# Optimization experiments

Measured on AMD Instinct MI355X. Metric: run time of the kernel, lower is better.

The kernel has to match this reference:

```python
import jax, jax.numpy as jnp
import numpy as np

B, T, E, U, V = 64, 100, 512, 512, 32000


def gru_layer(xs_tm, Wg, bg, Wc, bc):
    """TF GRUCell math. xs_tm: [T, B, D]. Returns (ys [T,B,U], h_final [B,U])."""
    u_dim = Wc.shape[1]
    h0 = jnp.zeros((xs_tm.shape[1], u_dim), xs_tm.dtype)

    def step(h, x):
        ru = jax.nn.sigmoid(jnp.concatenate([x, h], -1) @ Wg + bg)
        r, u = jnp.split(ru, 2, axis=-1)
        c = jnp.tanh(jnp.concatenate([x, r * h], -1) @ Wc + bc)
        h_new = u * h + (1.0 - u) * c
        return h_new, h_new

    h_final, ys = jax.lax.scan(step, h0, xs_tm)
    return ys, h_final


def setup_inputs() -> dict:
    key = jax.random.key(0)
    ks = jax.random.split(key, 16)

    def w(k, shape):
        fan_in = shape[0]
        return jax.random.normal(k, shape, jnp.float32) * (1.0 / np.sqrt(fan_in))

    inp = {
        "x": jax.random.randint(ks[0], (B, T), 0, V, jnp.int32),
        "embedding": jax.random.normal(ks[1], (V, E), jnp.float32) * 0.02,
        # bi-directional layer, input dim E
        "Wg_fw": w(ks[2], (E + U, 2 * U)), "bg_fw": jnp.ones((2 * U,), jnp.float32),
        "Wc_fw": w(ks[3], (E + U, U)),     "bc_fw": jnp.zeros((U,), jnp.float32),
        "Wg_bw": w(ks[4], (E + U, 2 * U)), "bg_bw": jnp.ones((2 * U,), jnp.float32),
        "Wc_bw": w(ks[5], (E + U, U)),     "bc_bw": jnp.zeros((U,), jnp.float32),
        # uni layer 1, input dim 2U (concat fw/bw)
        "Wg_u1": w(ks[6], (2 * U + U, 2 * U)), "bg_u1": jnp.ones((2 * U,), jnp.float32),
        "Wc_u1": w(ks[7], (2 * U + U, U)),     "bc_u1": jnp.zeros((U,), jnp.float32),
        # uni layer 2, input dim U
        "Wg_u2": w(ks[8], (U + U, 2 * U)), "bg_u2": jnp.ones((2 * U,), jnp.float32),
        "Wc_u2": w(ks[9], (U + U, U)),     "bc_u2": jnp.zeros((U,), jnp.float32),
    }
    return inp


def reference(x, embedding, Wg_fw, bg_fw, Wc_fw, bc_fw, Wg_bw, bg_bw, Wc_bw, bc_bw,
              Wg_u1, bg_u1, Wc_u1, bc_u1, Wg_u2, bg_u2, Wc_u2, bc_u2):
    emb = embedding[x]                      # [B, T, E] embedding lookup
    xs = jnp.swapaxes(emb, 0, 1)            # [T, B, E] time-major for scan
    # bidirectional GRU layer
    yf, _ = gru_layer(xs, Wg_fw, bg_fw, Wc_fw, bc_fw)
    yb, _ = gru_layer(xs[::-1], Wg_bw, bg_bw, Wc_bw, bc_bw)
    a = jnp.concatenate([yf, yb[::-1]], -1)  # [T, B, 2U]
    # 2-layer unidirectional GRU stack (MultiRNNCell)
    a, s1 = gru_layer(a, Wg_u1, bg_u1, Wc_u1, bc_u1)
    a, s2 = gru_layer(a, Wg_u2, bg_u2, Wc_u2, bc_u2)
    output = jnp.swapaxes(a, 0, 1)          # [B, T, U]
    state = jnp.stack([s1, s2])             # [2, B, U] per-layer final states
    return output, state
```

## Files before the change

### kernel.cpp

```cpp
#include <hip/hip_runtime.h>
#include <hip/hip_bf16.h>


#define TT 100

using f32x4 = __attribute__((ext_vector_type(4))) float;
using s16x8 = __attribute__((ext_vector_type(8))) short;
using u32x4 = __attribute__((ext_vector_type(4))) unsigned;

__device__ __forceinline__ unsigned short f2bfu(float x) {
  __hip_bfloat16 b = __float2bfloat16(x);
  unsigned short u;
  __builtin_memcpy(&u, &b, sizeof(u));
  return u;
}
__device__ __forceinline__ float bfu2f(unsigned short u) {
  __hip_bfloat16 b;
  __builtin_memcpy(&b, &u, sizeof(b));
  return __bfloat162float(b);
}
__device__ __forceinline__ float sigm(float x) {
  x = fminf(fmaxf(x, -30.f), 30.f);
  return 1.f / (1.f + __expf(-x));
}
__device__ __forceinline__ float tanh_fast(float x) {
  x = fminf(fmaxf(x, -15.f), 15.f);
  float e = __expf(-2.f * x);
  return (1.f - e) / (1.f + e);
}
__device__ __forceinline__ void vm_drain() {
  asm volatile("s_waitcnt vmcnt(0)" ::: "memory");
}
__device__ __forceinline__ void sc1_store_b16(void* p, unsigned v) {
  asm volatile("global_store_short %0, %1, off sc0 sc1" :: "v"(p), "v"(v) : "memory");
}

__global__ __launch_bounds__(256) void pack_w_kernel(const float* __restrict__ Wg,
                                                     const float* __restrict__ Wc,
                                                     int ldg, int ldc, int ktTot,
                                                     unsigned short* __restrict__ hi,
                                                     unsigned short* __restrict__ lo) {
  const int gg = blockIdx.x * 256 + threadIdx.x;
  if (gg >= 96 * ktTot * 64) return;
  const int lane = gg & 63;
  const int pair = gg >> 6;
  const int kt = pair % ktTot;
  const int nt = pair / ktTot;
  const int kg = lane >> 4;
  const int nl = lane & 15;
  const size_t off = (size_t)gg * 8;
  for (int i = 0; i < 8; ++i) {
    const int k = kt * 32 + kg * 8 + i;
    float v = (nt < 64) ? Wg[(size_t)k * ldg + nt * 16 + nl]
                        : Wc[(size_t)k * ldc + (nt - 64) * 16 + nl];
    unsigned short h = f2bfu(v);
    hi[off + i] = h;
    lo[off + i] = f2bfu(v - bfu2f(h));
  }
}

template <int ASRC>
__global__ __launch_bounds__(256) void gemm_mfma(
    const int* __restrict__ xtok, const float* __restrict__ emb,
    const unsigned short* __restrict__ aHi, const unsigned short* __restrict__ aLo, int lda,
    const unsigned short* __restrict__ bHi, const unsigned short* __restrict__ bLo,
    int ktTot, int ktX,
    const float* __restrict__ bg, const float* __restrict__ bc,
    float* __restrict__ C) {
  __shared__ unsigned short Ah[128 * 40];
  __shared__ unsigned short Al[128 * 40];

  const int tid = threadIdx.x;
  const int lane = tid & 63;
  const int w = tid >> 6;
  const int bm = blockIdx.x, bn = blockIdx.y;
  const int fm = lane & 15, fkg = lane >> 4;

  const int arow = tid >> 1;
  const int koff = (tid & 1) * 16;
  const int rowg = bm * 128 + arow;
  int embIdx = 0;
  if (ASRC == 0) {
    const int t_ = rowg >> 6, b_ = rowg & 63;
    embIdx = xtok[b_ * TT + t_];
  }

  f32x4 acc[2][8];
#pragma unroll
  for (int rt = 0; rt < 2; ++rt)
#pragma unroll
    for (int ni = 0; ni < 8; ++ni) acc[rt][ni] = (f32x4){0.f, 0.f, 0.f, 0.f};

  for (int kt = 0; kt < ktX; ++kt) {
    __syncthreads();
    if (ASRC == 0) {
      const float* src = emb + (size_t)embIdx * 512 + kt * 32 + koff;
      s16x8 h0, h1, l0, l1;
#pragma unroll
      for (int c = 0; c < 2; ++c) {
        f32x4 va = *(const f32x4*)(src + c * 8);
        f32x4 vb = *(const f32x4*)(src + c * 8 + 4);
        s16x8 hh, ll;
#pragma unroll
        for (int j = 0; j < 4; ++j) {
          unsigned short h = f2bfu(va[j]);
          hh[j] = (short)h; ll[j] = (short)f2bfu(va[j] - bfu2f(h));
          unsigned short h2 = f2bfu(vb[j]);
          hh[j + 4] = (short)h2; ll[j + 4] = (short)f2bfu(vb[j] - bfu2f(h2));
        }
        if (c == 0) { h0 = hh; l0 = ll; } else { h1 = hh; l1 = ll; }
      }
      *(s16x8*)(Ah + arow * 40 + koff) = h0;
      *(s16x8*)(Ah + arow * 40 + koff + 8) = h1;
      *(s16x8*)(Al + arow * 40 + koff) = l0;
      *(s16x8*)(Al + arow * 40 + koff + 8) = l1;
    } else {
      const size_t so = (size_t)rowg * lda + kt * 32 + koff;
      s16x8 h0 = *(const s16x8*)(aHi + so);
      s16x8 h1 = *(const s16x8*)(aHi + so + 8);
      s16x8 l0 = *(const s16x8*)(aLo + so);
      s16x8 l1 = *(const s16x8*)(aLo + so + 8);
      *(s16x8*)(Ah + arow * 40 + koff) = h0;
      *(s16x8*)(Ah + arow * 40 + koff + 8) = h1;
      *(s16x8*)(Al + arow * 40 + koff) = l0;
      *(s16x8*)(Al + arow * 40 + koff + 8) = l1;
    }
    __syncthreads();

    s16x8 ah[2], al[2];
#pragma unroll
    for (int rt = 0; rt < 2; ++rt) {
      const int m = w * 32 + rt * 16 + fm;
      ah[rt] = *(const s16x8*)(Ah + m * 40 + fkg * 8);
      al[rt] = *(const s16x8*)(Al + m * 40 + fkg * 8);
    }
#pragma unroll
    for (int ni = 0; ni < 8; ++ni) {
      const int nt = bn * 8 + ni;
      const size_t bo = ((size_t)nt * ktTot + kt) * 512 + lane * 8;
      s16x8 bh = *(const s16x8*)(bHi + bo);
      s16x8 bl = *(const s16x8*)(bLo + bo);
#pragma unroll
      for (int rt = 0; rt < 2; ++rt) {
        acc[rt][ni] = __builtin_amdgcn_mfma_f32_16x16x32_bf16(ah[rt], bh, acc[rt][ni], 0, 0, 0);
        acc[rt][ni] = __builtin_amdgcn_mfma_f32_16x16x32_bf16(ah[rt], bl, acc[rt][ni], 0, 0, 0);
        acc[rt][ni] = __builtin_amdgcn_mfma_f32_16x16x32_bf16(al[rt], bh, acc[rt][ni], 0, 0, 0);
      }
    }
  }

#pragma unroll
  for (int ni = 0; ni < 8; ++ni) {
    const int nt = bn * 8 + ni;
    int dcol; float bias;
    if (nt < 64) { dcol = nt * 16 + fm; bias = bg[dcol]; }
    else { dcol = 1024 + (nt - 64) * 16 + fm; bias = bc[(nt - 64) * 16 + fm]; }
#pragma unroll
    for (int rt = 0; rt < 2; ++rt)
#pragma unroll
      for (int j = 0; j < 4; ++j) {
        const int row = bm * 128 + w * 32 + rt * 16 + fkg * 4 + j;
        C[(size_t)row * 1536 + dcol] = acc[rt][ni][j] + bias;
      }
  }
}

template <int NB>
__global__ __launch_bounds__(256, 1) void gru_scan_kernel(
    const float* __restrict__ gxF, const float* __restrict__ gxB,
    const unsigned short* __restrict__ wHiF, const unsigned short* __restrict__ wLoF,
    const unsigned short* __restrict__ wHiB, const unsigned short* __restrict__ wLoB,
    int ktTot, int ktH0,
    unsigned* __restrict__ hPkG, unsigned* __restrict__ rPkG,
    unsigned* __restrict__ slots,
    unsigned short* __restrict__ yHi, unsigned short* __restrict__ yLo, int yld,
    float* __restrict__ outb,
    float* __restrict__ stout) {
  __shared__ unsigned short wHi_s[3 * 8192];
  __shared__ unsigned short wLo_s[3 * 8192];
  __shared__ float scr[4][16][17];
  __shared__ float scr2[4][16][17];

  const int tid = threadIdx.x;
  const int lane = tid & 63;
  const int wv = tid >> 6;
  const int bid = blockIdx.x;
  const int g = bid & 7;
  const int wg = bid >> 3;
  const int hs = wg << 4;

  int dir = 0, b0;
  const float* gx;
  const unsigned short *wph, *wpl;
  if (NB == 16) {
    dir = g & 1;
    b0 = (g >> 1) << 4;
    gx = dir ? gxB : gxF;
    wph = dir ? wHiB : wHiF;
    wpl = dir ? wLoB : wLoF;
  } else {
    b0 = g * NB;
    gx = gxF;
    wph = wHiF;
    wpl = wLoF;
  }

  {
    const int nt0[3] = {wg, 32 + wg, 64 + wg};
    for (int c = 0; c < 3; ++c) {
      const unsigned short* sH = wph + ((size_t)nt0[c] * ktTot + ktH0) * 512;
      const unsigned short* sL = wpl + ((size_t)nt0[c] * ktTot + ktH0) * 512;
      unsigned short* dH = wHi_s + c * 8192;
      unsigned short* dL = wLo_s + c * 8192;
#pragma unroll
      for (int it = 0; it < 4; ++it) {
        const int o = (it * 256 + tid) * 8;
        *(s16x8*)(dH + o) = *(const s16x8*)(sH + o);
        *(s16x8*)(dL + o) = *(const s16x8*)(sL + o);
      }
    }
  }
  __syncthreads();

  unsigned* gslots = slots + g * 32;

  const int fm = lane & 15;
  const int fkg = lane >> 4;
  const int afe = fm * 512;
  const int asw = (fm & 7) << 3;

  const int ob = tid >> 4, oj = tid & 15;
  const bool own = (ob < NB);
  const int ui = ob * 512 + ((hs + oj) ^ ((ob & 7) << 3));

  const size_t tileo = (size_t)g * 8192;

  auto mfma_regs = [&](int cidx, const s16x8* ah, const s16x8* al,
                       float (*dst)[16][17]) {
    f32x4 acc0 = {0.f, 0.f, 0.f, 0.f}, acc1 = {0.f, 0.f, 0.f, 0.f};
#pragma unroll
    for (int q = 0; q < 4; ++q) {
      const int kt = wv * 4 + q;
      const int wo = ((cidx * 16 + kt) * 64 + lane) * 8;
      s16x8 bh = *(const s16x8*)(wHi_s + wo);
      s16x8 bl = *(const s16x8*)(wLo_s + wo);
      if (q & 1) {
        acc1 = __builtin_amdgcn_mfma_f32_16x16x32_bf16(ah[q], bh, acc1, 0, 0, 0);
        acc1 = __builtin_amdgcn_mfma_f32_16x16x32_bf16(ah[q], bl, acc1, 0, 0, 0);
        acc1 = __builtin_amdgcn_mfma_f32_16x16x32_bf16(al[q], bh, acc1, 0, 0, 0);
      } else {
        acc0 = __builtin_amdgcn_mfma_f32_16x16x32_bf16(ah[q], bh, acc0, 0, 0, 0);
        acc0 = __builtin_amdgcn_mfma_f32_16x16x32_bf16(ah[q], bl, acc0, 0, 0, 0);
        acc0 = __builtin_amdgcn_mfma_f32_16x16x32_bf16(al[q], bh, acc0, 0, 0, 0);
      }
    }
#pragma unroll
    for (int j = 0; j < 4; ++j) dst[wv][fkg * 4 + j][fm] = acc0[j] + acc1[j];
  };

  auto load_frags = [&](const unsigned* pk, s16x8* ah, s16x8* al,
                        bool withHv, unsigned* hvOut) {
    u32x4 d[4][2];
#pragma unroll
    for (int q = 0; q < 4; ++q) {
      const int kt = wv * 4 + q;
      const unsigned* p = pk + tileo + afe + ((kt * 32 + fkg * 8) ^ asw);
      asm volatile("global_load_dwordx4 %0, %1, off sc0 sc1"
                   : "=v"(d[q][0]) : "v"(p) : "memory");
      asm volatile("global_load_dwordx4 %0, %1, off sc0 sc1"
                   : "=v"(d[q][1]) : "v"(p + 4) : "memory");
    }
    if (withHv && own)
      asm volatile("global_load_dword %0, %1, off sc0 sc1"
                   : "=v"(*hvOut) : "v"(pk + tileo + ui) : "memory");
    vm_drain();
    __builtin_amdgcn_sched_barrier(0);
#pragma unroll
    for (int q = 0; q < 4; ++q) {
      u32x4 hh, ll;
#pragma unroll
      for (int i = 0; i < 2; ++i) {
        const u32x4 dd = d[q][i];
        hh[2 * i] = (dd[0] & 0xffffu) | (dd[1] << 16);
        hh[2 * i + 1] = (dd[2] & 0xffffu) | (dd[3] << 16);
        ll[2 * i] = (dd[0] >> 16) | (dd[1] & 0xffff0000u);
        ll[2 * i + 1] = (dd[2] >> 16) | (dd[3] & 0xffff0000u);
      }
      __builtin_memcpy(&ah[q], &hh, 16);
      __builtin_memcpy(&al[q], &ll, 16);
    }
  };

  auto poll = [&](unsigned target) {
    if (tid < 32) {
      const unsigned* p = gslots + tid;
      unsigned v;
      do {
        asm volatile("global_load_dword %0, %1, off sc0 sc1\n\ts_waitcnt vmcnt(0)"
                     : "=v"(v) : "v"(p) : "memory");
      } while (!__all(v >= target));
    }
    __syncthreads();
  };

  float gxr = 0.f, gxu = 0.f, gxc = 0.f;
  if (own) {
    const float* row = gx + ((size_t)(dir ? TT - 1 : 0) * 64 + b0 + ob) * 1536 + hs + oj;
    gxr = row[0]; gxu = row[512]; gxc = row[1024];
  }

  for (int t = 0; t < TT; ++t) {
    const int tg = dir ? (TT - 1 - t) : t;

    s16x8 ah[4], al[4];
    unsigned hvu = 0;
    load_frags(hPkG, ah, al, true, &hvu);
    mfma_regs(0, ah, al, scr);
    __syncthreads();

    float hv = 0.f;
    if (own) {
      float rpre = scr[0][ob][oj] + scr[1][ob][oj] + scr[2][ob][oj] + scr[3][ob][oj] + gxr;
      float sg = sigm(rpre);
      hv = bfu2f((unsigned short)(hvu & 0xffffu)) + bfu2f((unsigned short)(hvu >> 16));
      float rh = sg * hv;
      unsigned short hh_ = f2bfu(rh);
      unsigned short ll_ = f2bfu(rh - bfu2f(hh_));
      unsigned e = (unsigned)hh_ | ((unsigned)ll_ << 16);
      asm volatile("global_store_dword %0, %1, off sc0 sc1"
                   :: "v"(rPkG + tileo + ui), "v"(e) : "memory");
    }
    vm_drain();
    __syncthreads();
    if (tid == 0) {
      unsigned tv = 2 * t + 1;
      asm volatile("global_store_dword %0, %1, off sc0 sc1"
                   :: "v"(gslots + wg), "v"(tv) : "memory");
    }

    mfma_regs(1, ah, al, scr2);

    float ngxr = 0.f, ngxu = 0.f, ngxc = 0.f;
    if (own && t + 1 < TT) {
      const int tgn = dir ? (TT - 2 - t) : (t + 1);
      const float* row = gx + ((size_t)tgn * 64 + b0 + ob) * 1536 + hs + oj;
      ngxr = row[0]; ngxu = row[512]; ngxc = row[1024];
    }

    poll(2 * t + 1);

    load_frags(rPkG, ah, al, false, nullptr);
    mfma_regs(2, ah, al, scr);
    __syncthreads();

    float hn = 0.f;
    unsigned short hh_ = 0, ll_ = 0;
    if (own) {
      float upre = scr2[0][ob][oj] + scr2[1][ob][oj] + scr2[2][ob][oj] + scr2[3][ob][oj] + gxu;
      float uv = sigm(upre);
      float cpre = scr[0][ob][oj] + scr[1][ob][oj] + scr[2][ob][oj] + scr[3][ob][oj] + gxc;
      float cv = tanh_fast(cpre);
      hn = uv * hv + (1.f - uv) * cv;
      hh_ = f2bfu(hn);
      ll_ = f2bfu(hn - bfu2f(hh_));
    }

    if (t == TT - 1) {
      if (own) {
        if (yHi) {
          const int ycol = (NB == 16) ? (dir * 512 + hs + oj) : (hs + oj);
          const size_t yi = ((size_t)tg * 64 + (b0 + ob)) * yld + ycol;
          yHi[yi] = hh_; yLo[yi] = ll_;
        }
        if (outb) outb[((size_t)(b0 + ob) * TT + t) * 512 + hs + oj] = hn;
        if (stout) stout[(size_t)(b0 + ob) * 512 + hs + oj] = hn;
      }
      break;
    }

    if (own) {
      unsigned e = (unsigned)hh_ | ((unsigned)ll_ << 16);
      asm volatile("global_store_dword %0, %1, off sc0 sc1"
                   :: "v"(hPkG + tileo + ui), "v"(e) : "memory");
    }
    vm_drain();
    __syncthreads();
    if (tid == 0) {
      unsigned tv = 2 * t + 2;
      asm volatile("global_store_dword %0, %1, off sc0 sc1"
                   :: "v"(gslots + wg), "v"(tv) : "memory");
    }

    if (own) {
      if (yHi) {
        const int ycol = (NB == 16) ? (dir * 512 + hs + oj) : (hs + oj);
        const size_t yi = ((size_t)tg * 64 + (b0 + ob)) * yld + ycol;
        yHi[yi] = hh_; yLo[yi] = ll_;
      }
      if (outb) outb[((size_t)(b0 + ob) * TT + t) * 512 + hs + oj] = hn;
    }
    gxr = ngxr; gxu = ngxu; gxc = ngxc;

    poll(2 * t + 2);
  }
}

__global__ __launch_bounds__(256, 1) void uni_fused_kernel(
    const float* __restrict__ gx1,
    const unsigned short* __restrict__ w1Hi, const unsigned short* __restrict__ w1Lo,
    const unsigned short* __restrict__ w2Hi, const unsigned short* __restrict__ w2Lo,
    const float* __restrict__ bg2, const float* __restrict__ bc2,
    unsigned* __restrict__ hPk1, unsigned* __restrict__ rPk1,
    unsigned* __restrict__ hPk2, unsigned* __restrict__ rPk2,
    unsigned* __restrict__ slots1, unsigned* __restrict__ slots2,
    unsigned short* __restrict__ y1Hi, unsigned short* __restrict__ y1Lo,
    float* __restrict__ out, float* __restrict__ st1, float* __restrict__ st2) {
  __shared__ unsigned short wHi_s[3 * 8192];
  __shared__ unsigned short wLo_s[3 * 8192];
  __shared__ float scr[4][16][17];
  __shared__ float scr2[4][16][17];
  __shared__ float scr3[4][16][17];

  const int tid = threadIdx.x;
  const int lane = tid & 63;
  const int wv = tid >> 6;
  const int bid = blockIdx.x;
  const int role = (bid >= 128);
  const int g = (bid & 127) >> 5;
  const int wg = bid & 31;
  const int hs = wg << 4;
  const int b0 = g * 16;

  const unsigned short* wph = role ? w2Hi : w1Hi;
  const unsigned short* wpl = role ? w2Lo : w1Lo;
  const int ktTot = role ? 32 : 48;
  const int ktH0 = role ? 16 : 32;
  unsigned* hPk = role ? hPk2 : hPk1;
  unsigned* rPk = role ? rPk2 : rPk1;
  unsigned* myslots = (role ? slots2 : slots1) + g * 32;
  unsigned* u1gs = slots1 + g * 32;

  {
    const int nt0[3] = {wg, 32 + wg, 64 + wg};
    for (int c = 0; c < 3; ++c) {
      const unsigned short* sH = wph + ((size_t)nt0[c] * ktTot + ktH0) * 512;
      const unsigned short* sL = wpl + ((size_t)nt0[c] * ktTot + ktH0) * 512;
      unsigned short* dH = wHi_s + c * 8192;
      unsigned short* dL = wLo_s + c * 8192;
#pragma unroll
      for (int it = 0; it < 4; ++it) {
        const int o = (it * 256 + tid) * 8;
        *(s16x8*)(dH + o) = *(const s16x8*)(sH + o);
        *(s16x8*)(dL + o) = *(const s16x8*)(sL + o);
      }
    }
  }
  __syncthreads();

  const int fm = lane & 15;
  const int fkg = lane >> 4;
  const int afe = fm * 512;
  const int asw = (fm & 7) << 3;
  const int ob = tid >> 4, oj = tid & 15;
  const int ui = ob * 512 + ((hs + oj) ^ ((ob & 7) << 3));
  const size_t tileo = (size_t)g * 8192;

  auto mfma_regs = [&](int cidx, const s16x8* ah, const s16x8* al,
                       float (*dst)[16][17]) {
    f32x4 acc0 = {0.f, 0.f, 0.f, 0.f}, acc1 = {0.f, 0.f, 0.f, 0.f};
#pragma unroll
    for (int q = 0; q < 4; ++q) {
      const int kt = wv * 4 + q;
      const int wo = ((cidx * 16 + kt) * 64 + lane) * 8;
      s16x8 bh = *(const s16x8*)(wHi_s + wo);
      s16x8 bl = *(const s16x8*)(wLo_s + wo);
      if (q & 1) {
        acc1 = __builtin_amdgcn_mfma_f32_16x16x32_bf16(ah[q], bh, acc1, 0, 0, 0);
        acc1 = __builtin_amdgcn_mfma_f32_16x16x32_bf16(ah[q], bl, acc1, 0, 0, 0);
        acc1 = __builtin_amdgcn_mfma_f32_16x16x32_bf16(al[q], bh, acc1, 0, 0, 0);
      } else {
        acc0 = __builtin_amdgcn_mfma_f32_16x16x32_bf16(ah[q], bh, acc0, 0, 0, 0);
        acc0 = __builtin_amdgcn_mfma_f32_16x16x32_bf16(ah[q], bl, acc0, 0, 0, 0);
        acc0 = __builtin_amdgcn_mfma_f32_16x16x32_bf16(al[q], bh, acc0, 0, 0, 0);
      }
    }
#pragma unroll
    for (int j = 0; j < 4; ++j) dst[wv][fkg * 4 + j][fm] = acc0[j] + acc1[j];
  };

  auto mfma_xp = [&](int cidx, const s16x8* ah, const s16x8* al,
                     float (*dst)[16][17]) {
    const int nt0[3] = {wg, 32 + wg, 64 + wg};
    f32x4 acc0 = {0.f, 0.f, 0.f, 0.f}, acc1 = {0.f, 0.f, 0.f, 0.f};
#pragma unroll
    for (int q = 0; q < 4; ++q) {
      const int kt = wv * 4 + q;
      const size_t bo = ((size_t)nt0[cidx] * 32 + kt) * 512 + lane * 8;
      s16x8 bh = *(const s16x8*)(w2Hi + bo);
      s16x8 bl = *(const s16x8*)(w2Lo + bo);
      if (q & 1) {
        acc1 = __builtin_amdgcn_mfma_f32_16x16x32_bf16(ah[q], bh, acc1, 0, 0, 0);
        acc1 = __builtin_amdgcn_mfma_f32_16x16x32_bf16(ah[q], bl, acc1, 0, 0, 0);
        acc1 = __builtin_amdgcn_mfma_f32_16x16x32_bf16(al[q], bh, acc1, 0, 0, 0);
      } else {
        acc0 = __builtin_amdgcn_mfma_f32_16x16x32_bf16(ah[q], bh, acc0, 0, 0, 0);
        acc0 = __builtin_amdgcn_mfma_f32_16x16x32_bf16(ah[q], bl, acc0, 0, 0, 0);
        acc0 = __builtin_amdgcn_mfma_f32_16x16x32_bf16(al[q], bh, acc0, 0, 0, 0);
      }
    }
#pragma unroll
    for (int j = 0; j < 4; ++j) dst[wv][fkg * 4 + j][fm] = acc0[j] + acc1[j];
  };

  auto load_frags = [&](const unsigned* pk, s16x8* ah, s16x8* al,
                        bool withHv, unsigned* hvOut) {
    u32x4 d[4][2];
#pragma unroll
    for (int q = 0; q < 4; ++q) {
      const int kt = wv * 4 + q;
      const unsigned* p = pk + tileo + afe + ((kt * 32 + fkg * 8) ^ asw);
      asm volatile("global_load_dwordx4 %0, %1, off sc0 sc1"
                   : "=v"(d[q][0]) : "v"(p) : "memory");
      asm volatile("global_load_dwordx4 %0, %1, off sc0 sc1"
                   : "=v"(d[q][1]) : "v"(p + 4) : "memory");
    }
    if (withHv)
      asm volatile("global_load_dword %0, %1, off sc0 sc1"
                   : "=v"(*hvOut) : "v"(pk + tileo + ui) : "memory");
    vm_drain();
    __builtin_amdgcn_sched_barrier(0);
#pragma unroll
    for (int q = 0; q < 4; ++q) {
      u32x4 hh, ll;
#pragma unroll
      for (int i = 0; i < 2; ++i) {
        const u32x4 dd = d[q][i];
        hh[2 * i] = (dd[0] & 0xffffu) | (dd[1] << 16);
        hh[2 * i + 1] = (dd[2] & 0xffffu) | (dd[3] << 16);
        ll[2 * i] = (dd[0] >> 16) | (dd[1] & 0xffff0000u);
        ll[2 * i + 1] = (dd[2] >> 16) | (dd[3] & 0xffff0000u);
      }
      __builtin_memcpy(&ah[q], &hh, 16);
      __builtin_memcpy(&al[q], &ll, 16);
    }
  };

  auto poll_arr = [&](const unsigned* arr, unsigned target) {
    if (tid < 32) {
      const unsigned* p = arr + tid;
      unsigned v;
      do {
        asm volatile("global_load_dword %0, %1, off sc0 sc1\n\ts_waitcnt vmcnt(0)"
                     : "=v"(v) : "v"(p) : "memory");
      } while (!__all(v >= target));
    }
    __syncthreads();
  };

  if (role == 0) {
    float gxr, gxu, gxc;
    {
      const float* row = gx1 + ((size_t)0 * 64 + b0 + ob) * 1536 + hs + oj;
      gxr = row[0]; gxu = row[512]; gxc = row[1024];
    }
    for (int t = 0; t < TT; ++t) {
      s16x8 ah[4], al[4];
      unsigned hvu = 0;
      load_frags(hPk, ah, al, true, &hvu);
      mfma_regs(0, ah, al, scr);
      __syncthreads();

      float rpre = scr[0][ob][oj] + scr[1][ob][oj] + scr[2][ob][oj] + scr[3][ob][oj] + gxr;
      float sg = sigm(rpre);
      float hv = bfu2f((unsigned short)(hvu & 0xffffu)) + bfu2f((unsigned short)(hvu >> 16));
      float rh = sg * hv;
      {
        unsigned short hh_ = f2bfu(rh);
        unsigned short ll_ = f2bfu(rh - bfu2f(hh_));
        unsigned e = (unsigned)hh_ | ((unsigned)ll_ << 16);
        asm volatile("global_store_dword %0, %1, off sc0 sc1"
                     :: "v"(rPk + tileo + ui), "v"(e) : "memory");
      }
      vm_drain();
      __syncthreads();
      if (tid == 0) {
        unsigned tv = 2 * t + 1;
        asm volatile("global_store_dword %0, %1, off sc0 sc1"
                     :: "v"(myslots + wg), "v"(tv) : "memory");
      }

      mfma_regs(1, ah, al, scr2);

      float ngxr = 0.f, ngxu = 0.f, ngxc = 0.f;
      if (t + 1 < TT) {
        const float* row = gx1 + ((size_t)(t + 1) * 64 + b0 + ob) * 1536 + hs + oj;
        ngxr = row[0]; ngxu = row[512]; ngxc = row[1024];
      }

      poll_arr(myslots, 2 * t + 1);

      load_frags(rPk, ah, al, false, nullptr);
      mfma_regs(2, ah, al, scr);
      __syncthreads();

      float upre = scr2[0][ob][oj] + scr2[1][ob][oj] + scr2[2][ob][oj] + scr2[3][ob][oj] + gxu;
      float uv = sigm(upre);
      float cpre = scr[0][ob][oj] + scr[1][ob][oj] + scr[2][ob][oj] + scr[3][ob][oj] + gxc;
      float hn = uv * hv + (1.f - uv) * tanh_fast(cpre);
      unsigned short hh_ = f2bfu(hn);
      unsigned short ll_ = f2bfu(hn - bfu2f(hh_));

      {
        const size_t yi = ((size_t)t * 64 + (b0 + ob)) * 512 + hs + oj;
        sc1_store_b16(y1Hi + yi, hh_);
        sc1_store_b16(y1Lo + yi, ll_);
      }
      if (t < TT - 1) {
        unsigned e = (unsigned)hh_ | ((unsigned)ll_ << 16);
        asm volatile("global_store_dword %0, %1, off sc0 sc1"
                     :: "v"(hPk + tileo + ui), "v"(e) : "memory");
      } else {
        st1[(size_t)(b0 + ob) * 512 + hs + oj] = hn;
      }
      vm_drain();
      __syncthreads();
      if (tid == 0) {
        unsigned tv = 2 * t + 2;
        asm volatile("global_store_dword %0, %1, off sc0 sc1"
                     :: "v"(myslots + wg), "v"(tv) : "memory");
      }
      if (t == TT - 1) break;
      gxr = ngxr; gxu = ngxu; gxc = ngxc;
      poll_arr(myslots, 2 * t + 2);
    }
  } else {
    const float br = bg2[hs + oj], bu = bg2[512 + hs + oj], bc_ = bc2[hs + oj];
    for (int t = 0; t < TT; ++t) {
      poll_arr(u1gs, 2 * t + 2);

      s16x8 xh[4], xl[4];
      {
#pragma unroll
        for (int q = 0; q < 4; ++q) {
          const int kt = wv * 4 + q;
          const size_t yo = ((size_t)t * 64 + b0 + fm) * 512 + kt * 32 + fkg * 8;
          asm volatile("global_load_dwordx4 %0, %1, off sc0 sc1"
                       : "=v"(xh[q]) : "v"(y1Hi + yo) : "memory");
          asm volatile("global_load_dwordx4 %0, %1, off sc0 sc1"
                       : "=v"(xl[q]) : "v"(y1Lo + yo) : "memory");
        }
        vm_drain();
        __builtin_amdgcn_sched_barrier(0);
      }
      mfma_xp(0, xh, xl, scr);
      mfma_xp(1, xh, xl, scr2);
      mfma_xp(2, xh, xl, scr3);
      __syncthreads();
      float gxr = scr[0][ob][oj] + scr[1][ob][oj] + scr[2][ob][oj] + scr[3][ob][oj] + br;
      float gxu = scr2[0][ob][oj] + scr2[1][ob][oj] + scr2[2][ob][oj] + scr2[3][ob][oj] + bu;
      float gxc = scr3[0][ob][oj] + scr3[1][ob][oj] + scr3[2][ob][oj] + scr3[3][ob][oj] + bc_;
      __syncthreads();

      s16x8 ah[4], al[4];
      unsigned hvu = 0;
      load_frags(hPk, ah, al, true, &hvu);
      mfma_regs(0, ah, al, scr);
      __syncthreads();

      float rpre = scr[0][ob][oj] + scr[1][ob][oj] + scr[2][ob][oj] + scr[3][ob][oj] + gxr;
      float sg = sigm(rpre);
      float hv = bfu2f((unsigned short)(hvu & 0xffffu)) + bfu2f((unsigned short)(hvu >> 16));
      float rh = sg * hv;
      {
        unsigned short hh_ = f2bfu(rh);
        unsigned short ll_ = f2bfu(rh - bfu2f(hh_));
        unsigned e = (unsigned)hh_ | ((unsigned)ll_ << 16);
        asm volatile("global_store_dword %0, %1, off sc0 sc1"
                     :: "v"(rPk + tileo + ui), "v"(e) : "memory");
      }
      vm_drain();
      __syncthreads();
      if (tid == 0) {
        unsigned tv = 2 * t + 1;
        asm volatile("global_store_dword %0, %1, off sc0 sc1"
                     :: "v"(myslots + wg), "v"(tv) : "memory");
      }

      mfma_regs(1, ah, al, scr2);
      poll_arr(myslots, 2 * t + 1);

      load_frags(rPk, ah, al, false, nullptr);
      mfma_regs(2, ah, al, scr);
      __syncthreads();

      float upre = scr2[0][ob][oj] + scr2[1][ob][oj] + scr2[2][ob][oj] + scr2[3][ob][oj] + gxu;
      float uv = sigm(upre);
      float cpre = scr[0][ob][oj] + scr[1][ob][oj] + scr[2][ob][oj] + scr[3][ob][oj] + gxc;
      float hn = uv * hv + (1.f - uv) * tanh_fast(cpre);

      if (t == TT - 1) {
        out[((size_t)(b0 + ob) * TT + t) * 512 + hs + oj] = hn;
        st2[(size_t)(b0 + ob) * 512 + hs + oj] = hn;
        break;
      }
      {
        unsigned short hh_ = f2bfu(hn);
        unsigned short ll_ = f2bfu(hn - bfu2f(hh_));
        unsigned e = (unsigned)hh_ | ((unsigned)ll_ << 16);
        asm volatile("global_store_dword %0, %1, off sc0 sc1"
                     :: "v"(hPk + tileo + ui), "v"(e) : "memory");
      }
      vm_drain();
      __syncthreads();
      if (tid == 0) {
        unsigned tv = 2 * t + 2;
        asm volatile("global_store_dword %0, %1, off sc0 sc1"
                     :: "v"(myslots + wg), "v"(tv) : "memory");
      }
      out[((size_t)(b0 + ob) * TT + t) * 512 + hs + oj] = hn;
      poll_arr(myslots, 2 * t + 2);
    }
  }
}

extern "C" void kernel_launch(void* const* d_in, const int* in_sizes, int n_in,
                              void* d_out, int out_size, void* d_ws, size_t ws_size,
                              hipStream_t stream) {
  (void)in_sizes; (void)n_in; (void)out_size; (void)ws_size;
  const int* x = (const int*)d_in[0];
  const float* emb = (const float*)d_in[1];
  const float* WgFw = (const float*)d_in[2];
  const float* bgFw = (const float*)d_in[3];
  const float* WcFw = (const float*)d_in[4];
  const float* bcFw = (const float*)d_in[5];
  const float* WgBw = (const float*)d_in[6];
  const float* bgBw = (const float*)d_in[7];
  const float* WcBw = (const float*)d_in[8];
  const float* bcBw = (const float*)d_in[9];
  const float* WgU1 = (const float*)d_in[10];
  const float* bgU1 = (const float*)d_in[11];
  const float* WcU1 = (const float*)d_in[12];
  const float* bcU1 = (const float*)d_in[13];
  const float* WgU2 = (const float*)d_in[14];
  const float* bgU2 = (const float*)d_in[15];
  const float* WcU2 = (const float*)d_in[16];
  const float* bcU2 = (const float*)d_in[17];

  char* ws = (char*)d_ws;
  float* bufA = (float*)(ws + 0);
  float* bufB = (float*)(ws + 39321600);
  unsigned short* ycatHi = (unsigned short*)(ws + 78643200);
  unsigned short* ycatLo = (unsigned short*)(ws + 91750400);
  unsigned short* y1Hi = (unsigned short*)(ws + 78643200);
  unsigned short* y1Lo = (unsigned short*)(ws + 85196800);
  unsigned short* wpFwHi = (unsigned short*)(ws + 104857600);
  unsigned short* wpFwLo = (unsigned short*)(ws + 108003328);
  unsigned short* wpBwHi = (unsigned short*)(ws + 111149056);
  unsigned short* wpBwLo = (unsigned short*)(ws + 114294784);
  unsigned short* wpU1Hi = (unsigned short*)(ws + 117440512);
  unsigned short* wpU1Lo = (unsigned short*)(ws + 122159104);
  unsigned short* wpU2Hi = (unsigned short*)(ws + 104857600);
  unsigned short* wpU2Lo = (unsigned short*)(ws + 108003328);
  unsigned* tiles = (unsigned*)(ws + 126877696);
  unsigned* bars = (unsigned*)(ws + 127401984);

  unsigned* hPkB = tiles;
  unsigned* rPkB = tiles + 65536;
  unsigned* hPk1 = tiles;
  unsigned* rPk1 = tiles + 32768;
  unsigned* hPk2 = tiles + 65536;
  unsigned* rPk2 = tiles + 98304;

  float* out = (float*)d_out;
  float* st1 = out + (size_t)64 * TT * 512;
  float* st2 = st1 + 64 * 512;

  hipMemsetAsync(bars, 0, 4096, stream);

  pack_w_kernel<<<768, 256, 0, stream>>>(WgFw, WcFw, 1024, 512, 32, wpFwHi, wpFwLo);
  pack_w_kernel<<<768, 256, 0, stream>>>(WgBw, WcBw, 1024, 512, 32, wpBwHi, wpBwLo);
  pack_w_kernel<<<1152, 256, 0, stream>>>(WgU1, WcU1, 1024, 512, 48, wpU1Hi, wpU1Lo);

  gemm_mfma<0><<<dim3(50, 12), 256, 0, stream>>>(
      x, emb, nullptr, nullptr, 0, wpFwHi, wpFwLo, 32, 16, bgFw, bcFw, bufA);
  gemm_mfma<0><<<dim3(50, 12), 256, 0, stream>>>(
      x, emb, nullptr, nullptr, 0, wpBwHi, wpBwLo, 32, 16, bgBw, bcBw, bufB);

  hipMemsetAsync(tiles, 0, 524288, stream);
  {
    const float *a0 = bufA, *a1 = bufB;
    const unsigned short *w0 = wpFwHi, *w1 = wpFwLo, *w2 = wpBwHi, *w3 = wpBwLo;
    int ktT = 32, ktH = 16;
    unsigned *h0 = hPkB, *r0 = rPkB;
    unsigned* bp = bars;
    unsigned short *yh = ycatHi, *yl = ycatLo; int yld = 1024;
    float *on = nullptr, *sn = nullptr;
    void* args[] = {&a0, &a1, &w0, &w1, &w2, &w3, &ktT, &ktH, &h0, &r0,
                    &bp, &yh, &yl, &yld, &on, &sn};
    hipLaunchCooperativeKernel((const void*)gru_scan_kernel<16>, dim3(256), dim3(256),
                               args, 0, stream);
  }

  pack_w_kernel<<<768, 256, 0, stream>>>(WgU2, WcU2, 1024, 512, 32, wpU2Hi, wpU2Lo);

  gemm_mfma<1><<<dim3(50, 12), 256, 0, stream>>>(
      nullptr, nullptr, ycatHi, ycatLo, 1024, wpU1Hi, wpU1Lo, 48, 32, bgU1, bcU1, bufA);

  hipMemsetAsync(tiles, 0, 524288, stream);
  {
    const float* a0 = bufA;
    const unsigned short *w0 = wpU1Hi, *w1 = wpU1Lo, *w2 = wpU2Hi, *w3 = wpU2Lo;
    const float *b2 = bgU2, *c2 = bcU2;
    unsigned *h1 = hPk1, *r1 = rPk1, *h2 = hPk2, *r2 = rPk2;
    unsigned *s1p = bars + 256, *s2p = bars + 384;
    unsigned short *yh = y1Hi, *yl = y1Lo;
    float *op = out, *t1 = st1, *t2 = st2;
    void* args[] = {&a0, &w0, &w1, &w2, &w3, &b2, &c2,
                    &h1, &r1, &h2, &r2, &s1p, &s2p, &yh, &yl, &op, &t1, &t2};
    hipLaunchCooperativeKernel((const void*)uni_fused_kernel, dim3(256), dim3(256),
                               args, 0, stream);
  }
}
```

Measured before the change: 1.591 ms.

## Fuse embedding input projections into bidirectional scan and pipeline layer-2 projections

Drops the two standalone input-projection GEMMs for the bidirectional layer. The scan kernel now gathers embedding rows, splits them to hi/lo bf16 and computes the x·W gate projections per timestep with MFMA, overlapping them with waits on the recurrent barrier. The layer-2 scan also moves its next-step input projection into the current step's barrier wait slots. This removes the large gx buffer traffic and two kernel launches, but adds MFMA work and global weight reads to the latency-critical serial loop, plus extra block syncs.

```diff
diff --git a/kernel.cpp b/kernel.cpp
--- a/kernel.cpp
+++ b/kernel.cpp
@@ -79,11 +79,6 @@
   const int arow = tid >> 1;
   const int koff = (tid & 1) * 16;
   const int rowg = bm * 128 + arow;
-  int embIdx = 0;
-  if (ASRC == 0) {
-    const int t_ = rowg >> 6, b_ = rowg & 63;
-    embIdx = xtok[b_ * TT + t_];
-  }
 
   f32x4 acc[2][8];
 #pragma unroll
@@ -93,28 +88,7 @@
 
   for (int kt = 0; kt < ktX; ++kt) {
     __syncthreads();
-    if (ASRC == 0) {
-      const float* src = emb + (size_t)embIdx * 512 + kt * 32 + koff;
-      s16x8 h0, h1, l0, l1;
-#pragma unroll
-      for (int c = 0; c < 2; ++c) {
-        f32x4 va = *(const f32x4*)(src + c * 8);
-        f32x4 vb = *(const f32x4*)(src + c * 8 + 4);
-        s16x8 hh, ll;
-#pragma unroll
-        for (int j = 0; j < 4; ++j) {
-          unsigned short h = f2bfu(va[j]);
-          hh[j] = (short)h; ll[j] = (short)f2bfu(va[j] - bfu2f(h));
-          unsigned short h2 = f2bfu(vb[j]);
-          hh[j + 4] = (short)h2; ll[j + 4] = (short)f2bfu(vb[j] - bfu2f(h2));
-        }
-        if (c == 0) { h0 = hh; l0 = ll; } else { h1 = hh; l1 = ll; }
-      }
-      *(s16x8*)(Ah + arow * 40 + koff) = h0;
-      *(s16x8*)(Ah + arow * 40 + koff + 8) = h1;
-      *(s16x8*)(Al + arow * 40 + koff) = l0;
-      *(s16x8*)(Al + arow * 40 + koff + 8) = l1;
-    } else {
+    {
       const size_t so = (size_t)rowg * lda + kt * 32 + koff;
       s16x8 h0 = *(const s16x8*)(aHi + so);
       s16x8 h1 = *(const s16x8*)(aHi + so + 8);
@@ -165,21 +139,20 @@
   }
 }
 
-template <int NB>
-__global__ __launch_bounds__(256, 1) void gru_scan_kernel(
-    const float* __restrict__ gxF, const float* __restrict__ gxB,
+__global__ __launch_bounds__(256, 1) void bidir_scan_kernel(
+    const int* __restrict__ xtok, const float* __restrict__ emb,
     const unsigned short* __restrict__ wHiF, const unsigned short* __restrict__ wLoF,
     const unsigned short* __restrict__ wHiB, const unsigned short* __restrict__ wLoB,
-    int ktTot, int ktH0,
+    const float* __restrict__ bgF, const float* __restrict__ bcF,
+    const float* __restrict__ bgB, const float* __restrict__ bcB,
     unsigned* __restrict__ hPkG, unsigned* __restrict__ rPkG,
     unsigned* __restrict__ slots,
-    unsigned short* __restrict__ yHi, unsigned short* __restrict__ yLo, int yld,
-    float* __restrict__ outb,
-    float* __restrict__ stout) {
+    unsigned short* __restrict__ yHi, unsigned short* __restrict__ yLo) {
   __shared__ unsigned short wHi_s[3 * 8192];
   __shared__ unsigned short wLo_s[3 * 8192];
   __shared__ float scr[4][16][17];
   __shared__ float scr2[4][16][17];
+  __shared__ float scr3[4][16][17];
 
   const int tid = threadIdx.x;
   const int lane = tid & 63;
@@ -188,28 +161,19 @@
   const int g = bid & 7;
   const int wg = bid >> 3;
   const int hs = wg << 4;
-
-  int dir = 0, b0;
-  const float* gx;
-  const unsigned short *wph, *wpl;
-  if (NB == 16) {
-    dir = g & 1;
-    b0 = (g >> 1) << 4;
-    gx = dir ? gxB : gxF;
-    wph = dir ? wHiB : wHiF;
-    wpl = dir ? wLoB : wLoF;
-  } else {
-    b0 = g * NB;
-    gx = gxF;
-    wph = wHiF;
-    wpl = wLoF;
-  }
+  const int dir = g & 1;
+  const int b0 = (g >> 1) << 4;
+
+  const unsigned short* wph = dir ? wHiB : wHiF;
+  const unsigned short* wpl = dir ? wLoB : wLoF;
+  const float* bgD = dir ? bgB : bgF;
+  const float* bcD = dir ? bcB : bcF;
 
   {
     const int nt0[3] = {wg, 32 + wg, 64 + wg};
     for (int c = 0; c < 3; ++c) {
-      const unsigned short* sH = wph + ((size_t)nt0[c] * ktTot + ktH0) * 512;
-      const unsigned short* sL = wpl + ((size_t)nt0[c] * ktTot + ktH0) * 512;
+      const unsigned short* sH = wph + ((size_t)nt0[c] * 32 + 16) * 512;
+      const unsigned short* sL = wpl + ((size_t)nt0[c] * 32 + 16) * 512;
       unsigned short* dH = wHi_s + c * 8192;
       unsigned short* dL = wLo_s + c * 8192;
 #pragma unroll
@@ -223,17 +187,14 @@
   __syncthreads();
 
   unsigned* gslots = slots + g * 32;
-
   const int fm = lane & 15;
   const int fkg = lane >> 4;
   const int afe = fm * 512;
   const int asw = (fm & 7) << 3;
-
   const int ob = tid >> 4, oj = tid & 15;
-  const bool own = (ob < NB);
   const int ui = ob * 512 + ((hs + oj) ^ ((ob & 7) << 3));
-
   const size_t tileo = (size_t)g * 8192;
+  const float br = bgD[hs + oj], bu = bgD[512 + hs + oj], bcv = bcD[hs + oj];
 
   auto mfma_regs = [&](int cidx, const s16x8* ah, const s16x8* al,
                        float (*dst)[16][17]) {
@@ -258,6 +219,50 @@
     for (int j = 0; j < 4; ++j) dst[wv][fkg * 4 + j][fm] = acc0[j] + acc1[j];
   };
 
+  auto mfma_xpg = [&](int nt, const s16x8* xh, const s16x8* xl,
+                      float (*dst)[16][17]) {
+    f32x4 acc0 = {0.f, 0.f, 0.f, 0.f}, acc1 = {0.f, 0.f, 0.f, 0.f};
+#pragma unroll
+    for (int q = 0; q < 4; ++q) {
+      const int kt = wv * 4 + q;
+      const size_t bo = ((size_t)nt * 32 + kt) * 512 + lane * 8;
+      s16x8 bh = *(const s16x8*)(wph + bo);
+      s16x8 bl = *(const s16x8*)(wpl + bo);
+      if (q & 1) {
+        acc1 = __builtin_amdgcn_mfma_f32_16x16x32_bf16(xh[q], bh, acc1, 0, 0, 0);
+        acc1 = __builtin_amdgcn_mfma_f32_16x16x32_bf16(xh[q], bl, acc1, 0, 0, 0);
+        acc1 = __builtin_amdgcn_mfma_f32_16x16x32_bf16(xl[q], bh, acc1, 0, 0, 0);
+      } else {
+        acc0 = __builtin_amdgcn_mfma_f32_16x16x32_bf16(xh[q], bh, acc0, 0, 0, 0);
+        acc0 = __builtin_amdgcn_mfma_f32_16x16x32_bf16(xh[q], bl, acc0, 0, 0, 0);
+        acc0 = __builtin_amdgcn_mfma_f32_16x16x32_bf16(xl[q], bh, acc0, 0, 0, 0);
+      }
+    }
+#pragma unroll
+    for (int j = 0; j < 4; ++j) dst[wv][fkg * 4 + j][fm] = acc0[j] + acc1[j];
+  };
+
+  auto load_emb_frags = [&](int tg, s16x8* xh, s16x8* xl) {
+    const int tok = xtok[(b0 + fm) * TT + tg];
+    const float* er = emb + (size_t)tok * 512;
+#pragma unroll
+    for (int q = 0; q < 4; ++q) {
+      const int kt = wv * 4 + q;
+      const float* p = er + kt * 32 + fkg * 8;
+      f32x4 a = *(const f32x4*)p;
+      f32x4 b = *(const f32x4*)(p + 4);
+      s16x8 hh, ll;
+#pragma unroll
+      for (int j = 0; j < 4; ++j) {
+        unsigned short h1 = f2bfu(a[j]);
+        hh[j] = (short)h1; ll[j] = (short)f2bfu(a[j] - bfu2f(h1));
+        unsigned short h2 = f2bfu(b[j]);
+        hh[j + 4] = (short)h2; ll[j + 4] = (short)f2bfu(b[j] - bfu2f(h2));
+      }
+      xh[q] = hh; xl[q] = ll;
+    }
+  };
+
   auto load_frags = [&](const unsigned* pk, s16x8* ah, s16x8* al,
                         bool withHv, unsigned* hvOut) {
     u32x4 d[4][2];
@@ -270,7 +275,7 @@
       asm volatile("global_load_dwordx4 %0, %1, off sc0 sc1"
                    : "=v"(d[q][1]) : "v"(p + 4) : "memory");
     }
-    if (withHv && own)
+    if (withHv)
       asm volatile("global_load_dword %0, %1, off sc0 sc1"
                    : "=v"(*hvOut) : "v"(pk + tileo + ui) : "memory");
     vm_drain();
@@ -303,12 +308,21 @@
     __syncthreads();
   };
 
-  float gxr = 0.f, gxu = 0.f, gxc = 0.f;
-  if (own) {
-    const float* row = gx + ((size_t)(dir ? TT - 1 : 0) * 64 + b0 + ob) * 1536 + hs + oj;
-    gxr = row[0]; gxu = row[512]; gxc = row[1024];
-  }
-
+  float gxr, gxu, gxc;
+  {
+    s16x8 xh0[4], xl0[4];
+    load_emb_frags(dir ? TT - 1 : 0, xh0, xl0);
+    mfma_xpg(wg, xh0, xl0, scr);
+    mfma_xpg(32 + wg, xh0, xl0, scr2);
+    mfma_xpg(64 + wg, xh0, xl0, scr3);
+    __syncthreads();
+    gxr = scr[0][ob][oj] + scr[1][ob][oj] + scr[2][ob][oj] + scr[3][ob][oj] + br;
+    gxu = scr2[0][ob][oj] + scr2[1][ob][oj] + scr2[2][ob][oj] + scr2[3][ob][oj] + bu;
+    gxc = scr3[0][ob][oj] + scr3[1][ob][oj] + scr3[2][ob][oj] + scr3[3][ob][oj] + bcv;
+    __syncthreads();
+  }
+
+  s16x8 xh[4], xl[4];
   for (int t = 0; t < TT; ++t) {
     const int tg = dir ? (TT - 1 - t) : t;
 
@@ -318,12 +332,11 @@
     mfma_regs(0, ah, al, scr);
     __syncthreads();
 
-    float hv = 0.f;
-    if (own) {
-      float rpre = scr[0][ob][oj] + scr[1][ob][oj] + scr[2][ob][oj] + scr[3][ob][oj] + gxr;
-      float sg = sigm(rpre);
-      hv = bfu2f((unsigned short)(hvu & 0xffffu)) + bfu2f((unsigned short)(hvu >> 16));
-      float rh = sg * hv;
+    float rpre = scr[0][ob][oj] + scr[1][ob][oj] + scr[2][ob][oj] + scr[3][ob][oj] + gxr;
+    float sg = sigm(rpre);
+    float hv = bfu2f((unsigned short)(hvu & 0xffffu)) + bfu2f((unsigned short)(hvu >> 16));
+    float rh = sg * hv;
+    {
       unsigned short hh_ = f2bfu(rh);
       unsigned short ll_ = f2bfu(rh - bfu2f(hh_));
       unsigned e = (unsigned)hh_ | ((unsigned)ll_ << 16);
@@ -339,12 +352,15 @@
     }
 
     mfma_regs(1, ah, al, scr2);
-
     float ngxr = 0.f, ngxu = 0.f, ngxc = 0.f;
-    if (own && t + 1 < TT) {
-      const int tgn = dir ? (TT - 2 - t) : (t + 1);
-      const float* row = gx + ((size_t)tgn * 64 + b0 + ob) * 1536 + hs + oj;
-      ngxr = row[0]; ngxu = row[512]; ngxc = row[1024];
+    if (t + 1 < TT) {
+      load_emb_frags(dir ? TT - 2 - t : t + 1, xh, xl);
+      mfma_xpg(32 + wg, xh, xl, scr);
+      mfma_xpg(64 + wg, xh, xl, scr3);
+      __syncthreads();
+      ngxu = scr[0][ob][oj] + scr[1][ob][oj] + scr[2][ob][oj] + scr[3][ob][oj] + bu;
+      ngxc = scr3[0][ob][oj] + scr3[1][ob][oj] + scr3[2][ob][oj] + scr3[3][ob][oj] + bcv;
+      __syncthreads();
     }
 
     poll(2 * t + 1);
@@ -353,32 +369,20 @@
     mfma_regs(2, ah, al, scr);
     __syncthreads();
 
-    float hn = 0.f;
-    unsigned short hh_ = 0, ll_ = 0;
-    if (own) {
-      float upre = scr2[0][ob][oj] + scr2[1][ob][oj] + scr2[2][ob][oj] + scr2[3][ob][oj] + gxu;
-      float uv = sigm(upre);
-      float cpre = scr[0][ob][oj] + scr[1][ob][oj] + scr[2][ob][oj] + scr[3][ob][oj] + gxc;
-      float cv = tanh_fast(cpre);
-      hn = uv * hv + (1.f - uv) * cv;
-      hh_ = f2bfu(hn);
-      ll_ = f2bfu(hn - bfu2f(hh_));
-    }
+    float upre = scr2[0][ob][oj] + scr2[1][ob][oj] + scr2[2][ob][oj] + scr2[3][ob][oj] + gxu;
+    float uv = sigm(upre);
+    float cpre = scr[0][ob][oj] + scr[1][ob][oj] + scr[2][ob][oj] + scr[3][ob][oj] + gxc;
+    float hn = uv * hv + (1.f - uv) * tanh_fast(cpre);
+    unsigned short hh_ = f2bfu(hn);
+    unsigned short ll_ = f2bfu(hn - bfu2f(hh_));
 
     if (t == TT - 1) {
-      if (own) {
-        if (yHi) {
-          const int ycol = (NB == 16) ? (dir * 512 + hs + oj) : (hs + oj);
-          const size_t yi = ((size_t)tg * 64 + (b0 + ob)) * yld + ycol;
-          yHi[yi] = hh_; yLo[yi] = ll_;
-        }
-        if (outb) outb[((size_t)(b0 + ob) * TT + t) * 512 + hs + oj] = hn;
-        if (stout) stout[(size_t)(b0 + ob) * 512 + hs + oj] = hn;
-      }
+      const size_t yi = ((size_t)tg * 64 + (b0 + ob)) * 1024 + dir * 512 + hs + oj;
+      yHi[yi] = hh_; yLo[yi] = ll_;
       break;
     }
 
-    if (own) {
+    {
       unsigned e = (unsigned)hh_ | ((unsigned)ll_ << 16);
       asm volatile("global_store_dword %0, %1, off sc0 sc1"
                    :: "v"(hPkG + tileo + ui), "v"(e) : "memory");
@@ -391,13 +395,14 @@
                    :: "v"(gslots + wg), "v"(tv) : "memory");
     }
 
-    if (own) {
-      if (yHi) {
-        const int ycol = (NB == 16) ? (dir * 512 + hs + oj) : (hs + oj);
-        const size_t yi = ((size_t)tg * 64 + (b0 + ob)) * yld + ycol;
-        yHi[yi] = hh_; yLo[yi] = ll_;
-      }
-      if (outb) outb[((size_t)(b0 + ob) * TT + t) * 512 + hs + oj] = hn;
+    {
+      const size_t yi = ((size_t)tg * 64 + (b0 + ob)) * 1024 + dir * 512 + hs + oj;
+      yHi[yi] = hh_; yLo[yi] = ll_;
+    }
+    {
+      mfma_xpg(wg, xh, xl, scr);
+      __syncthreads();
+      ngxr = scr[0][ob][oj] + scr[1][ob][oj] + scr[2][ob][oj] + scr[3][ob][oj] + br;
     }
     gxr = ngxr; gxu = ngxu; gxc = ngxc;
 
@@ -488,7 +493,7 @@
     for (int j = 0; j < 4; ++j) dst[wv][fkg * 4 + j][fm] = acc0[j] + acc1[j];
   };
 
-  auto mfma_xp = [&](int cidx, const s16x8* ah, const s16x8* al,
+  auto mfma_xp = [&](int cidx, const s16x8* xh, const s16x8* xl,
                      float (*dst)[16][17]) {
     const int nt0[3] = {wg, 32 + wg, 64 + wg};
     f32x4 acc0 = {0.f, 0.f, 0.f, 0.f}, acc1 = {0.f, 0.f, 0.f, 0.f};
@@ -499,17 +504,31 @@
       s16x8 bh = *(const s16x8*)(w2Hi + bo);
       s16x8 bl = *(const s16x8*)(w2Lo + bo);
       if (q & 1) {
-        acc1 = __builtin_amdgcn_mfma_f32_16x16x32_bf16(ah[q], bh, acc1, 0, 0, 0);
-        acc1 = __builtin_amdgcn_mfma_f32_16x16x32_bf16(ah[q], bl, acc1, 0, 0, 0);
-        acc1 = __builtin_amdgcn_mfma_f32_16x16x32_bf16(al[q], bh, acc1, 0, 0, 0);
+        acc1 = __builtin_amdgcn_mfma_f32_16x16x32_bf16(xh[q], bh, acc1, 0, 0, 0);
+        acc1 = __builtin_amdgcn_mfma_f32_16x16x32_bf16(xh[q], bl, acc1, 0, 0, 0);
+        acc1 = __builtin_amdgcn_mfma_f32_16x16x32_bf16(xl[q], bh, acc1, 0, 0, 0);
       } else {
-        acc0 = __builtin_amdgcn_mfma_f32_16x16x32_bf16(ah[q], bh, acc0, 0, 0, 0);
-        acc0 = __builtin_amdgcn_mfma_f32_16x16x32_bf16(ah[q], bl, acc0, 0, 0, 0);
-        acc0 = __builtin_amdgcn_mfma_f32_16x16x32_bf16(al[q], bh, acc0, 0, 0, 0);
+        acc0 = __builtin_amdgcn_mfma_f32_16x16x32_bf16(xh[q], bh, acc0, 0, 0, 0);
+        acc0 = __builtin_amdgcn_mfma_f32_16x16x32_bf16(xh[q], bl, acc0, 0, 0, 0);
+        acc0 = __builtin_amdgcn_mfma_f32_16x16x32_bf16(xl[q], bh, acc0, 0, 0, 0);
       }
     }
 #pragma unroll
     for (int j = 0; j < 4; ++j) dst[wv][fkg * 4 + j][fm] = acc0[j] + acc1[j];
+  };
+
+  auto load_y1_frags = [&](int t_, s16x8* xh, s16x8* xl) {
+#pragma unroll
+    for (int q = 0; q < 4; ++q) {
+      const int kt = wv * 4 + q;
+      const size_t yo = ((size_t)t_ * 64 + b0 + fm) * 512 + kt * 32 + fkg * 8;
+      asm volatile("global_load_dwordx4 %0, %1, off sc0 sc1"
+                   : "=v"(xh[q]) : "v"(y1Hi + yo) : "memory");
+      asm volatile("global_load_dwordx4 %0, %1, off sc0 sc1"
+                   : "=v"(xl[q]) : "v"(y1Lo + yo) : "memory");
+    }
+    vm_drain();
+    __builtin_amdgcn_sched_barrier(0);
   };
 
   auto load_frags = [&](const unsigned* pk, s16x8* ah, s16x8* al,
@@ -635,32 +654,21 @@
     }
   } else {
     const float br = bg2[hs + oj], bu = bg2[512 + hs + oj], bc_ = bc2[hs + oj];
-    for (int t = 0; t < TT; ++t) {
-      poll_arr(u1gs, 2 * t + 2);
-
-      s16x8 xh[4], xl[4];
-      {
-#pragma unroll
-        for (int q = 0; q < 4; ++q) {
-          const int kt = wv * 4 + q;
-          const size_t yo = ((size_t)t * 64 + b0 + fm) * 512 + kt * 32 + fkg * 8;
-          asm volatile("global_load_dwordx4 %0, %1, off sc0 sc1"
-                       : "=v"(xh[q]) : "v"(y1Hi + yo) : "memory");
-          asm volatile("global_load_dwordx4 %0, %1, off sc0 sc1"
-                       : "=v"(xl[q]) : "v"(y1Lo + yo) : "memory");
-        }
-        vm_drain();
-        __builtin_amdgcn_sched_barrier(0);
-      }
+    s16x8 xh[4], xl[4];
+    float gxr, gxu, gxc;
+    {
+      poll_arr(u1gs, 2);
+      load_y1_frags(0, xh, xl);
       mfma_xp(0, xh, xl, scr);
       mfma_xp(1, xh, xl, scr2);
       mfma_xp(2, xh, xl, scr3);
       __syncthreads();
-      float gxr = scr[0][ob][oj] + scr[1][ob][oj] + scr[2][ob][oj] + scr[3][ob][oj] + br;
-      float gxu = scr2[0][ob][oj] + scr2[1][ob][oj] + scr2[2][ob][oj] + scr2[3][ob][oj] + bu;
-      float gxc = scr3[0][ob][oj] + scr3[1][ob][oj] + scr3[2][ob][oj] + scr3[3][ob][oj] + bc_;
-      __syncthreads();
-
+      gxr = scr[0][ob][oj] + scr[1][ob][oj] + scr[2][ob][oj] + scr[3][ob][oj] + br;
+      gxu = scr2[0][ob][oj] + scr2[1][ob][oj] + scr2[2][ob][oj] + scr2[3][ob][oj] + bu;
+      gxc = scr3[0][ob][oj] + scr3[1][ob][oj] + scr3[2][ob][oj] + scr3[3][ob][oj] + bc_;
+      __syncthreads();
+    }
+    for (int t = 0; t < TT; ++t) {
       s16x8 ah[4], al[4];
       unsigned hvu = 0;
       load_frags(hPk, ah, al, true, &hvu);
@@ -687,6 +695,18 @@
       }
 
       mfma_regs(1, ah, al, scr2);
+      float ngxr = 0.f, ngxu = 0.f, ngxc = 0.f;
+      if (t + 1 < TT) {
+        poll_arr(u1gs, 2 * (t + 1) + 2);
+        load_y1_frags(t + 1, xh, xl);
+        mfma_xp(1, xh, xl, scr);
+        mfma_xp(2, xh, xl, scr3);
+        __syncthreads();
+        ngxu = scr[0][ob][oj] + scr[1][ob][oj] + scr[2][ob][oj] + scr[3][ob][oj] + bu;
+        ngxc = scr3[0][ob][oj] + scr3[1][ob][oj] + scr3[2][ob][oj] + scr3[3][ob][oj] + bc_;
+        __syncthreads();
+      }
+
       poll_arr(myslots, 2 * t + 1);
 
       load_frags(rPk, ah, al, false, nullptr);
@@ -717,7 +737,14 @@
         asm volatile("global_store_dword %0, %1, off sc0 sc1"
                      :: "v"(myslots + wg), "v"(tv) : "memory");
       }
+
       out[((size_t)(b0 + ob) * TT + t) * 512 + hs + oj] = hn;
+      {
+        mfma_xp(0, xh, xl, scr);
+        __syncthreads();
+        ngxr = scr[0][ob][oj] + scr[1][ob][oj] + scr[2][ob][oj] + scr[3][ob][oj] + br;
+      }
+      gxr = ngxr; gxu = ngxu; gxc = ngxc;
       poll_arr(myslots, 2 * t + 2);
     }
   }
@@ -748,7 +775,6 @@
 
   char* ws = (char*)d_ws;
   float* bufA = (float*)(ws + 0);
-  float* bufB = (float*)(ws + 39321600);
   unsigned short* ycatHi = (unsigned short*)(ws + 78643200);
   unsigned short* ycatLo = (unsigned short*)(ws + 91750400);
   unsigned short* y1Hi = (unsigned short*)(ws + 78643200);
@@ -781,23 +807,18 @@
   pack_w_kernel<<<768, 256, 0, stream>>>(WgBw, WcBw, 1024, 512, 32, wpBwHi, wpBwLo);
   pack_w_kernel<<<1152, 256, 0, stream>>>(WgU1, WcU1, 1024, 512, 48, wpU1Hi, wpU1Lo);
 
-  gemm_mfma<0><<<dim3(50, 12), 256, 0, stream>>>(
-      x, emb, nullptr, nullptr, 0, wpFwHi, wpFwLo, 32, 16, bgFw, bcFw, bufA);
-  gemm_mfma<0><<<dim3(50, 12), 256, 0, stream>>>(
-      x, emb, nullptr, nullptr, 0, wpBwHi, wpBwLo, 32, 16, bgBw, bcBw, bufB);
-
   hipMemsetAsync(tiles, 0, 524288, stream);
   {
-    const float *a0 = bufA, *a1 = bufB;
+    const int* xt = x;
+    const float* em = emb;
     const unsigned short *w0 = wpFwHi, *w1 = wpFwLo, *w2 = wpBwHi, *w3 = wpBwLo;
-    int ktT = 32, ktH = 16;
+    const float *bF = bgFw, *cF = bcFw, *bB = bgBw, *cB = bcBw;
     unsigned *h0 = hPkB, *r0 = rPkB;
     unsigned* bp = bars;
-    unsigned short *yh = ycatHi, *yl = ycatLo; int yld = 1024;
-    float *on = nullptr, *sn = nullptr;
-    void* args[] = {&a0, &a1, &w0, &w1, &w2, &w3, &ktT, &ktH, &h0, &r0,
-                    &bp, &yh, &yl, &yld, &on, &sn};
-    hipLaunchCooperativeKernel((const void*)gru_scan_kernel<16>, dim3(256), dim3(256),
+    unsigned short *yh = ycatHi, *yl = ycatLo;
+    void* args[] = {&xt, &em, &w0, &w1, &w2, &w3, &bF, &cF, &bB, &cB,
+                    &h0, &r0, &bp, &yh, &yl};
+    hipLaunchCooperativeKernel((const void*)bidir_scan_kernel, dim3(256), dim3(256),
                                args, 0, stream);
   }
 
```

Measured after the change: 1.555 ms (median of 2 runs). -2.3%, faster.
